# Optimization experiments

Measured on AMD Instinct MI355X. Metric: run time of the kernel, lower is better.

The kernel has to match this reference:

```python
import jax, jax.numpy as jnp
import numpy as np

N, E, IN, HID, HEADS, EDIM, LAT = 10000, 160000, 20, 256, 4, 3, 1024


def gat(x, ei, ea, W, a_src, a_dst, We, a_e, b, H, C):
    # PyG GATConv, eval mode. ei: [2,E], ea: [E,edge_dim]
    n = x.shape[0]
    s, d = ei[0], ei[1]
    # add_self_loops with fill_value='mean': self-loop attr = mean of incoming edge attrs
    cnt = jax.ops.segment_sum(jnp.ones_like(s, jnp.float32), d, num_segments=n)
    loop_ea = jax.ops.segment_sum(ea, d, num_segments=n) / jnp.maximum(cnt, 1.0)[:, None]
    ar = jnp.arange(n, dtype=s.dtype)
    s = jnp.concatenate([s, ar])
    d = jnp.concatenate([d, ar])
    ea = jnp.concatenate([ea, loop_ea], axis=0)
    h = (x @ W).reshape(n, H, C)                       # [n,H,C]
    al_s = jnp.einsum('nhc,hc->nh', h, a_src)
    al_d = jnp.einsum('nhc,hc->nh', h, a_dst)
    e = (ea @ We).reshape(-1, H, C)                    # [E',H,C]
    al_e = jnp.einsum('ehc,hc->eh', e, a_e)
    alpha = jax.nn.leaky_relu(al_s[s] + al_d[d] + al_e, 0.2)  # [E',H]
    m = jax.ops.segment_max(alpha, d, num_segments=n)
    ex = jnp.exp(alpha - m[d])
    ssum = jax.ops.segment_sum(ex, d, num_segments=n)
    alpha = ex / (ssum[d] + 1e-16)
    out = jax.ops.segment_sum(h[s] * alpha[:, :, None], d, num_segments=n)
    return out.reshape(n, H * C) + b


def ln(x, g, b, eps=1e-5):
    m = x.mean(-1, keepdims=True)
    v = ((x - m) ** 2).mean(-1, keepdims=True)
    return g * (x - m) / jnp.sqrt(v + eps) + b


def setup_inputs() -> dict:
    key = jax.random.key(0)
    ks = jax.random.split(key, 16)
    sc = 0.05
    HC = HID * HEADS  # 1024
    return {
        'x': jax.random.normal(ks[0], (N, IN), jnp.float32),
        'edge_attr': jax.random.normal(ks[1], (E, EDIM), jnp.float32),
        'W1': jax.random.normal(ks[2], (IN, HC), jnp.float32) * sc,
        'a_src1': jax.random.normal(ks[3], (HEADS, HID), jnp.float32) * sc,
        'a_dst1': jax.random.normal(ks[4], (HEADS, HID), jnp.float32) * sc,
        'We1': jax.random.normal(ks[5], (EDIM, HC), jnp.float32) * sc,
        'a_e1': jax.random.normal(ks[6], (HEADS, HID), jnp.float32) * sc,
        'b1': jnp.zeros((HC,), jnp.float32),
        'g1': jnp.ones((HC,), jnp.float32),
        'be1': jnp.zeros((HC,), jnp.float32),
        'W2': jax.random.normal(ks[7], (HC, HID), jnp.float32) * sc,
        'a_src2': jax.random.normal(ks[8], (1, HID), jnp.float32) * sc,
        'a_dst2': jax.random.normal(ks[9], (1, HID), jnp.float32) * sc,
        'We2': jax.random.normal(ks[10], (EDIM, HID), jnp.float32) * sc,
        'a_e2': jax.random.normal(ks[11], (1, HID), jnp.float32) * sc,
        'b2': jnp.zeros((HID,), jnp.float32),
        'g2': jnp.ones((HID,), jnp.float32),
        'be2': jnp.zeros((HID,), jnp.float32),
        'Wfc': jax.random.normal(ks[12], (2 * HID, LAT), jnp.float32) * sc,
        'bfc': jnp.zeros((LAT,), jnp.float32),
        'gf': jnp.ones((LAT,), jnp.float32),
        'bf': jnp.zeros((LAT,), jnp.float32),
        'edge_index': jax.random.randint(ks[13], (2, E), 0, N, jnp.int32),
    }


def reference(x, edge_attr, W1, a_src1, a_dst1, We1, a_e1, b1, g1, be1,
              W2, a_src2, a_dst2, We2, a_e2, b2, g2, be2,
              Wfc, bfc, gf, bf, edge_index):
    h = jax.nn.elu(gat(x, edge_index, edge_attr, W1, a_src1, a_dst1, We1, a_e1, b1, HEADS, HID))
    h = ln(h, g1, be1)
    h = jax.nn.elu(gat(h, edge_index, edge_attr, W2, a_src2, a_dst2, We2, a_e2, b2, 1, HID))
    h = ln(h, g2, be2)
    x_mean = h.mean(axis=0)   # global_mean_pool, batch all zeros
    x_max = h.max(axis=0)     # global_max_pool
    g = jnp.concatenate([x_mean, x_max])[None, :]  # [1, 2*HID]
    out = ln(jax.nn.relu(g @ Wfc + bfc), gf, bf)   # [1, LAT]
    return out
```

## Files before the change

### kernel.cpp

```cpp
#include <hip/hip_runtime.h>
#include <hip/hip_bf16.h>

#define NN   10000
#define NE   160000
#define NEP  170000
#define IND  20
#define HIDD 256
#define NH   4
#define HCD  1024
#define LATD 1024
#define MPAD 10112
#define NREP 128

typedef __attribute__((ext_vector_type(8))) short short8v;
typedef __attribute__((ext_vector_type(4))) float f32x4;

__device__ __forceinline__ unsigned pk2(float a, float b) {
    union { __hip_bfloat16 h; unsigned short s; } x, y;
    x.h = __float2bfloat16(a); y.h = __float2bfloat16(b);
    return (unsigned)x.s | ((unsigned)y.s << 16);
}

__device__ __forceinline__ float block_reduce_sum1(float v, float* sm) {
    #pragma unroll
    for (int o = 32; o > 0; o >>= 1) v += __shfl_xor(v, o, 64);
    int wid = threadIdx.x >> 6, lane = threadIdx.x & 63, nw = blockDim.x >> 6;
    if (lane == 0) sm[wid] = v;
    __syncthreads();
    float r = 0.f;
    for (int i = 0; i < nw; i++) r += sm[i];
    __syncthreads();
    return r;
}

__device__ __forceinline__ void block_reduce_sum4(float* v, float* sm) {
    #pragma unroll
    for (int h = 0; h < 4; h++) {
        #pragma unroll
        for (int o = 32; o > 0; o >>= 1) v[h] += __shfl_xor(v[h], o, 64);
    }
    int wid = threadIdx.x >> 6, lane = threadIdx.x & 63, nw = blockDim.x >> 6;
    if (lane == 0) {
        sm[wid*4+0] = v[0]; sm[wid*4+1] = v[1]; sm[wid*4+2] = v[2]; sm[wid*4+3] = v[3];
    }
    __syncthreads();
    float r[4] = {0.f, 0.f, 0.f, 0.f};
    for (int i = 0; i < nw; i++) {
        r[0] += sm[i*4+0]; r[1] += sm[i*4+1]; r[2] += sm[i*4+2]; r[3] += sm[i*4+3];
    }
    __syncthreads();
    v[0] = r[0]; v[1] = r[1]; v[2] = r[2]; v[3] = r[3];
}

__global__ void k_prep(const float* __restrict__ W1, const float* __restrict__ as1,
                       const float* __restrict__ ad1, const float* __restrict__ We1,
                       const float* __restrict__ ae1, const float* __restrict__ We2,
                       const float* __restrict__ ae2, const float* __restrict__ W2,
                       float* __restrict__ prm, __hip_bfloat16* __restrict__ Bt,
                       __hip_bfloat16* __restrict__ w1b) {
    int bid = blockIdx.x, t = threadIdx.x;
    if (bid < 64) {
        __shared__ float sm[64][65];
        int k0 = (bid & 15) * 64, c0 = (bid >> 4) * 64;
        #pragma unroll
        for (int i = 0; i < 16; i++) {
            int idx = i * 256 + t;
            int r = idx >> 6, c = idx & 63;
            sm[r][c] = W2[(size_t)(k0 + r) * 256 + c0 + c];
        }
        __syncthreads();
        int c = t >> 2, kq = t & 3;
        unsigned int out[8];
        #pragma unroll
        for (int j = 0; j < 8; j++)
            out[j] = pk2(sm[kq * 16 + 2*j][c], sm[kq * 16 + 2*j + 1][c]);
        unsigned int* dst = (unsigned int*)(Bt + (size_t)(c0 + c) * 1024 + k0 + kq * 16);
        *(uint4*)dst = make_uint4(out[0], out[1], out[2], out[3]);
        *(uint4*)(dst + 4) = make_uint4(out[4], out[5], out[6], out[7]);
    } else if (bid == 64) {
        if (t < 80) {
            int i = t >> 2, h = t & 3; float s = 0.f;
            for (int c = 0; c < HIDD; c++) s += W1[i*HCD + h*HIDD + c] * as1[h*HIDD + c];
            prm[t] = s;
        } else if (t < 160) {
            int u = t - 80; int i = u >> 2, h = u & 3; float s = 0.f;
            for (int c = 0; c < HIDD; c++) s += W1[i*HCD + h*HIDD + c] * ad1[h*HIDD + c];
            prm[t] = s;
        } else if (t < 172) {
            int u = t - 160; int j = u >> 2, h = u & 3; float s = 0.f;
            for (int c = 0; c < HIDD; c++) s += We1[j*HCD + h*HIDD + c] * ae1[h*HIDD + c];
            prm[t] = s;
        } else if (t < 175) {
            int j = t - 172; float s = 0.f;
            for (int c = 0; c < HIDD; c++) s += We2[j*HIDD + c] * ae2[c];
            prm[t] = s;
        }
    } else {
        int base = (bid - 65) * 2560;
        #pragma unroll
        for (int r = 0; r < 10; r++) {
            int id = base + r * 256 + t;
            w1b[id] = __float2bfloat16(W1[id]);
        }
    }
}

__global__ void k_pre1(const int* __restrict__ ei, const float* __restrict__ ea,
                       const float* __restrict__ x, const float* __restrict__ prm,
                       float* __restrict__ cnt, float* __restrict__ lea3,
                       float* __restrict__ al1) {
    int e = blockIdx.x * 256 + threadIdx.x;
    if (e < NE) {
        int d = ei[NE + e];
        atomicAdd(&cnt[d], 1.0f);
        atomicAdd(&lea3[d*3+0], ea[e*3+0]);
        atomicAdd(&lea3[d*3+1], ea[e*3+1]);
        atomicAdd(&lea3[d*3+2], ea[e*3+2]);
    }
    if (e < NN) {
        int v = e;
        float xr[IND];
        #pragma unroll
        for (int i = 0; i < IND; i++) xr[i] = x[v * IND + i];
        #pragma unroll
        for (int h = 0; h < NH; h++) {
            float s = 0.f, d2 = 0.f;
            #pragma unroll
            for (int i = 0; i < IND; i++) { s += xr[i] * prm[i*4 + h]; d2 += xr[i] * prm[80 + i*4 + h]; }
            al1[v*8 + h] = s;
            al1[v*8 + 4 + h] = d2;
        }
    }
}

__global__ void k_scan(const float* __restrict__ cnt, int* __restrict__ offs) {
    __shared__ int sm[1024];
    int t = threadIdx.x;
    int base = t * 10;
    int loc[10]; int s = 0;
    if (t < 1000) {
        #pragma unroll
        for (int i = 0; i < 10; i++) { loc[i] = s; s += (int)cnt[base + i] + 1; }
    }
    sm[t] = (t < 1000) ? s : 0;
    __syncthreads();
    for (int o = 1; o < 1024; o <<= 1) {
        int x = (t >= o) ? sm[t - o] : 0;
        __syncthreads();
        sm[t] += x;
        __syncthreads();
    }
    int pre = (t > 0) ? sm[t - 1] : 0;
    if (t < 1000) {
        #pragma unroll
        for (int i = 0; i < 10; i++) offs[base + i] = pre + loc[i];
    }
    if (t == 1023) offs[NN] = sm[1023];
}

__global__ void k_edge1(const int* __restrict__ ei, const float* __restrict__ ea,
                        const float* __restrict__ cnt, const float* __restrict__ lea3,
                        const float* __restrict__ al1, const float* __restrict__ prm,
                        const int* __restrict__ offs, int* __restrict__ fill1,
                        int* __restrict__ csrs, float* __restrict__ cex1,
                        float* __restrict__ elog2) {
    int e = blockIdx.x * 256 + threadIdx.x;
    if (e >= NEP) return;
    int s, d; float e0, e1, e2;
    if (e < NE) {
        s = ei[e]; d = ei[NE + e];
        e0 = ea[e*3]; e1 = ea[e*3+1]; e2 = ea[e*3+2];
    } else {
        int v = e - NE; s = v; d = v;
        float ic = 1.f / fmaxf(cnt[v], 1.0f);
        e0 = lea3[v*3] * ic; e1 = lea3[v*3+1] * ic; e2 = lea3[v*3+2] * ic;
    }
    int slot = offs[d] + atomicAdd(&fill1[d], 1);
    csrs[slot] = s;
    elog2[slot] = e0*prm[172] + e1*prm[173] + e2*prm[174];
    float ex[4];
    #pragma unroll
    for (int h = 0; h < NH; h++) {
        float le = e0 * prm[160 + h] + e1 * prm[164 + h] + e2 * prm[168 + h];
        float lg = al1[s*8 + h] + al1[d*8 + 4 + h] + le;
        lg = lg > 0.f ? lg : 0.2f * lg;
        ex[h] = expf(lg);
    }
    *(float4*)(cex1 + (size_t)slot * 4) = make_float4(ex[0], ex[1], ex[2], ex[3]);
}

__global__ void __launch_bounds__(256)
k_agg1y(const int* __restrict__ offs, const int* __restrict__ csrs,
        const float* __restrict__ cex1, const float* __restrict__ x,
        const __hip_bfloat16* __restrict__ w1b, const float* __restrict__ b1,
        const float* __restrict__ g1, const float* __restrict__ be1,
        __hip_bfloat16* __restrict__ h1b) {
    __shared__ float xsn[4][NH][20];
    __shared__ float smr[16];
    int t = threadIdx.x, l = t & 63, n0 = t >> 6;
    int v4 = blockIdx.x * 4;
    {
        int v = v4 + n0;
        int beg = offs[v], end = offs[v + 1];
        int e = l >> 3, fs = l & 7;
        float acc[4][3] = {{0.f,0.f,0.f},{0.f,0.f,0.f},{0.f,0.f,0.f},{0.f,0.f,0.f}};
        float psa[4] = {0.f, 0.f, 0.f, 0.f};
        for (int j0 = beg; j0 < end; j0 += 8) {
            int jl = j0 + e;
            bool valid = jl < end;
            int s = csrs[valid ? jl : beg];
            float4 a4 = valid ? *(const float4*)(cex1 + (size_t)jl * 4)
                              : make_float4(0.f, 0.f, 0.f, 0.f);
            psa[0] += a4.x; psa[1] += a4.y; psa[2] += a4.z; psa[3] += a4.w;
            #pragma unroll
            for (int k = 0; k < 3; k++) {
                int fi = fs * 3 + k;
                float xv = (fi < IND) ? x[(size_t)s * IND + fi] : 0.f;
                acc[0][k] += a4.x * xv; acc[1][k] += a4.y * xv;
                acc[2][k] += a4.z * xv; acc[3][k] += a4.w * xv;
            }
        }
        #pragma unroll
        for (int o = 8; o <= 32; o <<= 1) {
            #pragma unroll
            for (int h = 0; h < 4; h++) {
                psa[h] += __shfl_xor(psa[h], o, 64);
                #pragma unroll
                for (int k = 0; k < 3; k++) acc[h][k] += __shfl_xor(acc[h][k], o, 64);
            }
        }
        if (e == 0) {
            #pragma unroll
            for (int h = 0; h < 4; h++) {
                float inv = 1.f / (psa[h] + 1e-16f);
                #pragma unroll
                for (int k = 0; k < 3; k++) {
                    int fi = fs * 3 + k;
                    if (fi < IND) xsn[n0][h][fi] = acc[h][k] * inv;
                }
            }
        }
    }
    __syncthreads();
    int hh = t >> 6;
    float vv[4][4] = {{0.f,0.f,0.f,0.f},{0.f,0.f,0.f,0.f},{0.f,0.f,0.f,0.f},{0.f,0.f,0.f,0.f}};
    #pragma unroll
    for (int i = 0; i < IND; i++) {
        uint2 wd = *(const uint2*)(w1b + (size_t)i * HCD + 4 * t);
        float w0 = __uint_as_float(wd.x << 16);
        float w1 = __uint_as_float(wd.x & 0xffff0000u);
        float w2 = __uint_as_float(wd.y << 16);
        float w3 = __uint_as_float(wd.y & 0xffff0000u);
        #pragma unroll
        for (int n = 0; n < 4; n++) {
            float xi = xsn[n][hh][i];
            vv[n][0] += xi * w0; vv[n][1] += xi * w1;
            vv[n][2] += xi * w2; vv[n][3] += xi * w3;
        }
    }
    float4 bb = ((const float4*)b1)[t];
    float ls[4];
    #pragma unroll
    for (int n = 0; n < 4; n++) {
        float s0, s1, s2, s3;
        s0 = vv[n][0] + bb.x; s0 = s0 > 0.f ? s0 : expm1f(s0);
        s1 = vv[n][1] + bb.y; s1 = s1 > 0.f ? s1 : expm1f(s1);
        s2 = vv[n][2] + bb.z; s2 = s2 > 0.f ? s2 : expm1f(s2);
        s3 = vv[n][3] + bb.w; s3 = s3 > 0.f ? s3 : expm1f(s3);
        vv[n][0] = s0; vv[n][1] = s1; vv[n][2] = s2; vv[n][3] = s3;
        ls[n] = s0 + s1 + s2 + s3;
    }
    block_reduce_sum4(ls, smr);
    float mu[4], q2[4];
    #pragma unroll
    for (int n = 0; n < 4; n++) {
        mu[n] = ls[n] * (1.f / 1024.f);
        float d0 = vv[n][0]-mu[n], d1 = vv[n][1]-mu[n], d2 = vv[n][2]-mu[n], d3 = vv[n][3]-mu[n];
        q2[n] = d0*d0 + d1*d1 + d2*d2 + d3*d3;
    }
    block_reduce_sum4(q2, smr);
    float4 gg = ((const float4*)g1)[t];
    float4 ee = ((const float4*)be1)[t];
    #pragma unroll
    for (int n = 0; n < 4; n++) {
        float rstd = rsqrtf(q2[n] * (1.f / 1024.f) + 1e-5f);
        float y0 = gg.x * (vv[n][0] - mu[n]) * rstd + ee.x;
        float y1 = gg.y * (vv[n][1] - mu[n]) * rstd + ee.y;
        float y2 = gg.z * (vv[n][2] - mu[n]) * rstd + ee.z;
        float y3 = gg.w * (vv[n][3] - mu[n]) * rstd + ee.w;
        *(uint2*)(h1b + (size_t)(v4 + n) * HCD + 4 * t) = make_uint2(pk2(y0, y1), pk2(y2, y3));
    }
}

__global__ void __launch_bounds__(256)
k_gemm2m(const __hip_bfloat16* __restrict__ A, const __hip_bfloat16* __restrict__ Bt,
         __hip_bfloat16* __restrict__ h2b) {
    __shared__ uint4 As4[256];
    char* As = (char*)As4;
    int t = threadIdx.x, l = t & 63, w = t >> 6;
    int m0 = blockIdx.x * 32;
    int srow = t >> 3, skc = t & 7;
    const __hip_bfloat16* gA = A + (size_t)(m0 + srow) * 1024 + skc * 8;
    int wbyte = (srow * 128 + skc * 16) ^ ((srow & 7) << 4);
    int r0 = l & 15, g = l >> 4;
    int ra[2][2];
    #pragma unroll
    for (int m = 0; m < 2; m++)
        #pragma unroll
        for (int kk = 0; kk < 2; kk++) {
            int r = r0 + m * 16;
            ra[m][kk] = (r * 128 + kk * 64 + g * 16) ^ ((r & 7) << 4);
        }
    const __hip_bfloat16* gB = Bt + (size_t)(w * 64 + r0) * 1024 + g * 8;
    f32x4 acc[2][4];
    #pragma unroll
    for (int m = 0; m < 2; m++)
        #pragma unroll
        for (int n = 0; n < 4; n++) acc[m][n] = (f32x4){0.f,0.f,0.f,0.f};
    uint4 sreg = *(const uint4*)gA;
    for (int it = 0; it < 16; ++it) {
        *(uint4*)(As + wbyte) = sreg;
        __syncthreads();
        if (it < 15) sreg = *(const uint4*)(gA + (it + 1) * 64);
        int k0 = it * 64;
        short8v bfr[4][2];
        #pragma unroll
        for (int n = 0; n < 4; n++)
            #pragma unroll
            for (int kk = 0; kk < 2; kk++)
                bfr[n][kk] = *(const short8v*)(gB + (size_t)n * 16 * 1024 + k0 + kk * 32);
        short8v afr[2][2];
        #pragma unroll
        for (int m = 0; m < 2; m++)
            #pragma unroll
            for (int kk = 0; kk < 2; kk++)
                afr[m][kk] = *(const short8v*)(As + ra[m][kk]);
        #pragma unroll
        for (int kk = 0; kk < 2; kk++)
            #pragma unroll
            for (int m = 0; m < 2; m++)
                #pragma unroll
                for (int n = 0; n < 4; n++)
                    acc[m][n] = __builtin_amdgcn_mfma_f32_16x16x32_bf16(afr[m][kk], bfr[n][kk], acc[m][n], 0, 0, 0);
        __syncthreads();
    }
    #pragma unroll
    for (int m = 0; m < 2; m++) {
        #pragma unroll
        for (int r = 0; r < 4; r++) {
            int row = m0 + m * 16 + g * 4 + r;
            if (row < NN) {
                #pragma unroll
                for (int n = 0; n < 4; n++) {
                    int col = w * 64 + n * 16 + r0;
                    h2b[(size_t)row * HIDD + col] = __float2bfloat16(acc[m][n][r]);
                }
            }
        }
    }
}

__global__ void __launch_bounds__(256)
k_al2(const __hip_bfloat16* __restrict__ h2b, const float* __restrict__ as2,
      const float* __restrict__ ad2, float* __restrict__ al2) {
    int l = threadIdx.x & 63;
    int v = blockIdx.x * 4 + (threadIdx.x >> 6);
    uint2 p = ((const uint2*)h2b)[(size_t)v * 64 + l];
    float f0 = __uint_as_float(p.x << 16), f1 = __uint_as_float(p.x & 0xffff0000u);
    float f2 = __uint_as_float(p.y << 16), f3 = __uint_as_float(p.y & 0xffff0000u);
    float4 sa = ((const float4*)as2)[l];
    float4 da = ((const float4*)ad2)[l];
    float s = f0*sa.x + f1*sa.y + f2*sa.z + f3*sa.w;
    float d = f0*da.x + f1*da.y + f2*da.z + f3*da.w;
    #pragma unroll
    for (int o = 1; o <= 32; o <<= 1) { s += __shfl_xor(s, o, 64); d += __shfl_xor(d, o, 64); }
    if (l == 0) { al2[v*2] = s; al2[v*2+1] = d; }
}

__global__ void __launch_bounds__(256)
k_agg2y(const int* __restrict__ offs, const int* __restrict__ csrs,
        const float* __restrict__ elog2, const float* __restrict__ al2,
        const __hip_bfloat16* __restrict__ h2b, const float* __restrict__ b2,
        const float* __restrict__ g2, const float* __restrict__ be2,
        float* __restrict__ gsum, unsigned* __restrict__ gmaxU) {
    __shared__ float sal[128];
    __shared__ int   ssr[128];
    __shared__ float sred[16];
    int t = threadIdx.x;
    int v = blockIdx.x;
    int beg = offs[v], end = offs[v + 1];
    float ald = al2[2 * v + 1];
    float acc = 0.f, ps = 0.f;
    for (int j0 = beg; j0 < end; j0 += 128) {
        int nb = end - j0; if (nb > 128) nb = 128;
        __syncthreads();
        if (t < 128) {
            int jl = j0 + t;
            float wv = 0.f; int s = 0;
            if (jl < end) {
                s = csrs[jl];
                float lg = al2[2 * s] + ald + elog2[jl];
                lg = lg > 0.f ? lg : 0.2f * lg;
                wv = expf(lg);
            }
            sal[t] = wv; ssr[t] = s;
            ps += wv;
        }
        __syncthreads();
        int nbr = (nb + 3) & ~3;
        for (int u = 0; u < nbr; u += 4) {
            float a0 = sal[u], a1 = sal[u+1], a2 = sal[u+2], a3 = sal[u+3];
            int s0 = ssr[u], s1 = ssr[u+1], s2 = ssr[u+2], s3 = ssr[u+3];
            float h0 = __bfloat162float(h2b[(size_t)s0 * HIDD + t]);
            float h1 = __bfloat162float(h2b[(size_t)s1 * HIDD + t]);
            float h2 = __bfloat162float(h2b[(size_t)s2 * HIDD + t]);
            float h3 = __bfloat162float(h2b[(size_t)s3 * HIDD + t]);
            acc += a0*h0 + a1*h1 + a2*h2 + a3*h3;
        }
    }
    float pst = block_reduce_sum1(ps, sred);
    float inv = 1.f / (pst + 1e-16f);
    float vf = acc * inv + b2[t];
    vf = vf > 0.f ? vf : expm1f(vf);
    float mu = block_reduce_sum1(vf, sred) * (1.f / 256.f);
    float dv = vf - mu;
    float var = block_reduce_sum1(dv * dv, sred) * (1.f / 256.f);
    float rstd = rsqrtf(var + 1e-5f);
    float outv = g2[t] * dv * rstd + be2[t];
    int rep = blockIdx.x & (NREP - 1);
    atomicAdd(&gsum[rep * 256 + t], outv);
    unsigned b = __float_as_uint(outv);
    unsigned k = (b & 0x80000000u) ? ~b : (b | 0x80000000u);
    atomicMax(&gmaxU[rep * 256 + t], k);
}

__global__ void k_gvec(const float* __restrict__ gsum, const unsigned* __restrict__ gmaxU,
                       float* __restrict__ gvec) {
    int t = threadIdx.x;
    float s = 0.f; unsigned km = 0u;
    for (int r = 0; r < NREP; r++) {
        s += gsum[r * 256 + t];
        unsigned k = gmaxU[r * 256 + t];
        km = k > km ? k : km;
    }
    gvec[t] = s * (1.f / (float)NN);
    unsigned b = (km & 0x80000000u) ? (km & 0x7fffffffu) : ~km;
    gvec[256 + t] = __uint_as_float(b);
}

__global__ void k_fc(const float* __restrict__ gvec, const float* __restrict__ Wfc,
                     float* __restrict__ fcacc) {
    int t = threadIdx.x;
    int kc = blockIdx.x >> 2;
    int c = (blockIdx.x & 3) * 256 + t;
    int r0 = kc * 64;
    float acc = 0.f;
    #pragma unroll 8
    for (int i = 0; i < 64; i++) acc += gvec[r0 + i] * Wfc[(size_t)(r0 + i) * LATD + c];
    atomicAdd(&fcacc[c], acc);
}

__global__ void k_out(const float* __restrict__ fcacc, const float* __restrict__ bfc,
                      const float* __restrict__ gf, const float* __restrict__ bf,
                      float* __restrict__ outp) {
    __shared__ float sm[16];
    int t = threadIdx.x;
    float v = fmaxf(fcacc[t] + bfc[t], 0.f);
    float mu = block_reduce_sum1(v, sm) * (1.f / 1024.f);
    float dv = v - mu;
    float var = block_reduce_sum1(dv * dv, sm) * (1.f / 1024.f);
    float rstd = rsqrtf(var + 1e-5f);
    outp[t] = gf[t] * dv * rstd + bf[t];
}

extern "C" void kernel_launch(void* const* d_in, const int* in_sizes, int n_in,
                              void* d_out, int out_size, void* d_ws, size_t ws_size,
                              hipStream_t stream) {
    const float* x      = (const float*)d_in[0];
    const float* ea     = (const float*)d_in[1];
    const float* W1     = (const float*)d_in[2];
    const float* a_src1 = (const float*)d_in[3];
    const float* a_dst1 = (const float*)d_in[4];
    const float* We1    = (const float*)d_in[5];
    const float* a_e1   = (const float*)d_in[6];
    const float* b1     = (const float*)d_in[7];
    const float* g1     = (const float*)d_in[8];
    const float* be1    = (const float*)d_in[9];
    const float* W2     = (const float*)d_in[10];
    const float* a_src2 = (const float*)d_in[11];
    const float* a_dst2 = (const float*)d_in[12];
    const float* We2    = (const float*)d_in[13];
    const float* a_e2   = (const float*)d_in[14];
    const float* b2     = (const float*)d_in[15];
    const float* g2     = (const float*)d_in[16];
    const float* be2    = (const float*)d_in[17];
    const float* Wfc    = (const float*)d_in[18];
    const float* bfc    = (const float*)d_in[19];
    const float* gf     = (const float*)d_in[20];
    const float* bf     = (const float*)d_in[21];
    const int*   ei     = (const int*)d_in[22];
    float* outp = (float*)d_out;

    char* p = (char*)d_ws;
    auto alloc = [&](size_t bytes) -> char* {
        char* r = p;
        p += (bytes + 255) & ~(size_t)255;
        return r;
    };
    float* cnt     = (float*)alloc((size_t)NN * 4);
    float* lea3    = (float*)alloc((size_t)NN * 3 * 4);
    int*   fill1   = (int*)  alloc((size_t)NN * 4);
    float* gsum    = (float*)alloc((size_t)NREP * 256 * 4);
    unsigned* gmaxU= (unsigned*)alloc((size_t)NREP * 256 * 4);
    float* fcacc   = (float*)alloc(1024 * 4);
    size_t zbytes  = (size_t)((char*)fcacc + 1024*4 - (char*)cnt);
    float* prm     = (float*)alloc(256 * 4);
    float* al1     = (float*)alloc((size_t)NN * 8 * 4);
    float* al2     = (float*)alloc((size_t)NN * 2 * 4);
    int*   offs    = (int*)  alloc((size_t)(NN + 1) * 4);
    int*   csrs    = (int*)  alloc((size_t)NEP * 4);
    float* cex1    = (float*)alloc((size_t)NEP * 4 * 4);
    float* elog2   = (float*)alloc((size_t)NEP * 4);
    __hip_bfloat16* w1b = (__hip_bfloat16*)alloc((size_t)IND * HCD * 2);
    __hip_bfloat16* h1b = (__hip_bfloat16*)alloc((size_t)MPAD * HCD * 2);
    __hip_bfloat16* w2t = (__hip_bfloat16*)alloc((size_t)HIDD * HCD * 2);
    __hip_bfloat16* h2b = (__hip_bfloat16*)alloc((size_t)NN * HIDD * 2);
    float* gvec    = (float*)alloc(512 * 4);

    hipMemsetAsync(cnt, 0, zbytes, stream);

    k_prep<<<73, 256, 0, stream>>>(W1, a_src1, a_dst1, We1, a_e1, We2, a_e2, W2,
                                   prm, w2t, w1b);
    k_pre1<<<(NE + 255) / 256, 256, 0, stream>>>(ei, ea, x, prm, cnt, lea3, al1);
    k_scan<<<1, 1024, 0, stream>>>(cnt, offs);
    k_edge1<<<(NEP + 255) / 256, 256, 0, stream>>>(ei, ea, cnt, lea3, al1, prm, offs,
                                                   fill1, csrs, cex1, elog2);
    k_agg1y<<<NN / 4, 256, 0, stream>>>(offs, csrs, cex1, x, w1b, b1, g1, be1, h1b);
    k_gemm2m<<<313, 256, 0, stream>>>(h1b, w2t, h2b);
    k_al2<<<NN / 4, 256, 0, stream>>>(h2b, a_src2, a_dst2, al2);
    k_agg2y<<<NN, 256, 0, stream>>>(offs, csrs, elog2, al2, h2b, b2, g2, be2,
                                    gsum, gmaxU);
    k_gvec<<<1, 256, 0, stream>>>(gsum, gmaxU, gvec);
    k_fc<<<32, 256, 0, stream>>>(gvec, Wfc, fcacc);
    k_out<<<1, 1024, 0, stream>>>(fcacc, bfc, gf, bf, outp);
}
```

Measured before the change: 305.5 us.

## Fuse small kernels and move layer-1 projection to MFMA with one-pass LayerNorm

```diff
diff --git a/kernel.cpp b/kernel.cpp
--- a/kernel.cpp
+++ b/kernel.cpp
@@ -21,6 +21,12 @@
     return (unsigned)x.s | ((unsigned)y.s << 16);
 }
 
+__device__ __forceinline__ unsigned short bf16bits(float a) {
+    union { __hip_bfloat16 h; unsigned short s; } x;
+    x.h = __float2bfloat16(a);
+    return x.s;
+}
+
 __device__ __forceinline__ float block_reduce_sum1(float v, float* sm) {
     #pragma unroll
     for (int o = 32; o > 0; o >>= 1) v += __shfl_xor(v, o, 64);
@@ -33,31 +39,14 @@
     return r;
 }
 
-__device__ __forceinline__ void block_reduce_sum4(float* v, float* sm) {
-    #pragma unroll
-    for (int h = 0; h < 4; h++) {
-        #pragma unroll
-        for (int o = 32; o > 0; o >>= 1) v[h] += __shfl_xor(v[h], o, 64);
-    }
-    int wid = threadIdx.x >> 6, lane = threadIdx.x & 63, nw = blockDim.x >> 6;
-    if (lane == 0) {
-        sm[wid*4+0] = v[0]; sm[wid*4+1] = v[1]; sm[wid*4+2] = v[2]; sm[wid*4+3] = v[3];
-    }
-    __syncthreads();
-    float r[4] = {0.f, 0.f, 0.f, 0.f};
-    for (int i = 0; i < nw; i++) {
-        r[0] += sm[i*4+0]; r[1] += sm[i*4+1]; r[2] += sm[i*4+2]; r[3] += sm[i*4+3];
-    }
-    __syncthreads();
-    v[0] = r[0]; v[1] = r[1]; v[2] = r[2]; v[3] = r[3];
-}
-
-__global__ void k_prep(const float* __restrict__ W1, const float* __restrict__ as1,
-                       const float* __restrict__ ad1, const float* __restrict__ We1,
-                       const float* __restrict__ ae1, const float* __restrict__ We2,
-                       const float* __restrict__ ae2, const float* __restrict__ W2,
-                       float* __restrict__ prm, __hip_bfloat16* __restrict__ Bt,
-                       __hip_bfloat16* __restrict__ w1b) {
+__global__ void k_front(const float* __restrict__ W1, const float* __restrict__ as1,
+                        const float* __restrict__ ad1, const float* __restrict__ We1,
+                        const float* __restrict__ ae1, const float* __restrict__ We2,
+                        const float* __restrict__ ae2, const float* __restrict__ W2,
+                        const int* __restrict__ ei, const float* __restrict__ ea,
+                        float* __restrict__ prm, __hip_bfloat16* __restrict__ Bt,
+                        __hip_bfloat16* __restrict__ w1t,
+                        float* __restrict__ cnt, float* __restrict__ lea3) {
     int bid = blockIdx.x, t = threadIdx.x;
     if (bid < 64) {
         __shared__ float sm[64][65];
@@ -95,67 +84,69 @@
             for (int c = 0; c < HIDD; c++) s += We2[j*HIDD + c] * ae2[c];
             prm[t] = s;
         }
+    } else if (bid < 73) {
+        int f = (bid - 65) * 128 + (t >> 1);
+        int half = t & 1;
+        #pragma unroll
+        for (int kk = 0; kk < 16; kk++) {
+            int k = half * 16 + kk;
+            float v = (k < IND) ? W1[(size_t)k * HCD + f] : 0.f;
+            w1t[(size_t)f * 32 + k] = __float2bfloat16(v);
+        }
     } else {
-        int base = (bid - 65) * 2560;
-        #pragma unroll
-        for (int r = 0; r < 10; r++) {
-            int id = base + r * 256 + t;
-            w1b[id] = __float2bfloat16(W1[id]);
-        }
-    }
-}
-
-__global__ void k_pre1(const int* __restrict__ ei, const float* __restrict__ ea,
-                       const float* __restrict__ x, const float* __restrict__ prm,
-                       float* __restrict__ cnt, float* __restrict__ lea3,
+        int e = (bid - 73) * 256 + t;
+        if (e < NE) {
+            int d = ei[NE + e];
+            atomicAdd(&cnt[d], 1.0f);
+            atomicAdd(&lea3[d*3+0], ea[e*3+0]);
+            atomicAdd(&lea3[d*3+1], ea[e*3+1]);
+            atomicAdd(&lea3[d*3+2], ea[e*3+2]);
+        }
+    }
+}
+
+__global__ void k_scan(const float* __restrict__ cnt, const float* __restrict__ x,
+                       const float* __restrict__ prm, int* __restrict__ offs,
                        float* __restrict__ al1) {
-    int e = blockIdx.x * 256 + threadIdx.x;
-    if (e < NE) {
-        int d = ei[NE + e];
-        atomicAdd(&cnt[d], 1.0f);
-        atomicAdd(&lea3[d*3+0], ea[e*3+0]);
-        atomicAdd(&lea3[d*3+1], ea[e*3+1]);
-        atomicAdd(&lea3[d*3+2], ea[e*3+2]);
-    }
-    if (e < NN) {
-        int v = e;
-        float xr[IND];
-        #pragma unroll
-        for (int i = 0; i < IND; i++) xr[i] = x[v * IND + i];
-        #pragma unroll
-        for (int h = 0; h < NH; h++) {
-            float s = 0.f, d2 = 0.f;
-            #pragma unroll
-            for (int i = 0; i < IND; i++) { s += xr[i] * prm[i*4 + h]; d2 += xr[i] * prm[80 + i*4 + h]; }
-            al1[v*8 + h] = s;
-            al1[v*8 + 4 + h] = d2;
-        }
-    }
-}
-
-__global__ void k_scan(const float* __restrict__ cnt, int* __restrict__ offs) {
-    __shared__ int sm[1024];
-    int t = threadIdx.x;
-    int base = t * 10;
-    int loc[10]; int s = 0;
-    if (t < 1000) {
-        #pragma unroll
-        for (int i = 0; i < 10; i++) { loc[i] = s; s += (int)cnt[base + i] + 1; }
-    }
-    sm[t] = (t < 1000) ? s : 0;
-    __syncthreads();
-    for (int o = 1; o < 1024; o <<= 1) {
-        int x = (t >= o) ? sm[t - o] : 0;
+    if (blockIdx.x == 0) {
+        __shared__ int sm[1024];
+        int t = threadIdx.x;
+        int base = t * 10;
+        int loc[10]; int s = 0;
+        if (t < 1000) {
+            #pragma unroll
+            for (int i = 0; i < 10; i++) { loc[i] = s; s += (int)cnt[base + i] + 1; }
+        }
+        sm[t] = (t < 1000) ? s : 0;
         __syncthreads();
-        sm[t] += x;
-        __syncthreads();
-    }
-    int pre = (t > 0) ? sm[t - 1] : 0;
-    if (t < 1000) {
-        #pragma unroll
-        for (int i = 0; i < 10; i++) offs[base + i] = pre + loc[i];
-    }
-    if (t == 1023) offs[NN] = sm[1023];
+        for (int o = 1; o < 1024; o <<= 1) {
+            int xv = (t >= o) ? sm[t - o] : 0;
+            __syncthreads();
+            sm[t] += xv;
+            __syncthreads();
+        }
+        int pre = (t > 0) ? sm[t - 1] : 0;
+        if (t < 1000) {
+            #pragma unroll
+            for (int i = 0; i < 10; i++) offs[base + i] = pre + loc[i];
+        }
+        if (t == 1023) offs[NN] = sm[1023];
+    } else {
+        int v = (blockIdx.x - 1) * 1024 + threadIdx.x;
+        if (v < NN) {
+            float xr[IND];
+            #pragma unroll
+            for (int i = 0; i < IND; i++) xr[i] = x[v * IND + i];
+            #pragma unroll
+            for (int h = 0; h < NH; h++) {
+                float s = 0.f, d2 = 0.f;
+                #pragma unroll
+                for (int i = 0; i < IND; i++) { s += xr[i] * prm[i*4 + h]; d2 += xr[i] * prm[80 + i*4 + h]; }
+                al1[v*8 + h] = s;
+                al1[v*8 + 4 + h] = d2;
+            }
+        }
+    }
 }
 
 __global__ void k_edge1(const int* __restrict__ ei, const float* __restrict__ ea,
@@ -184,28 +175,30 @@
         float le = e0 * prm[160 + h] + e1 * prm[164 + h] + e2 * prm[168 + h];
         float lg = al1[s*8 + h] + al1[d*8 + 4 + h] + le;
         lg = lg > 0.f ? lg : 0.2f * lg;
-        ex[h] = expf(lg);
+        ex[h] = __expf(lg);
     }
     *(float4*)(cex1 + (size_t)slot * 4) = make_float4(ex[0], ex[1], ex[2], ex[3]);
 }
 
 __global__ void __launch_bounds__(256)
-k_agg1y(const int* __restrict__ offs, const int* __restrict__ csrs,
-        const float* __restrict__ cex1, const float* __restrict__ x,
-        const __hip_bfloat16* __restrict__ w1b, const float* __restrict__ b1,
-        const float* __restrict__ g1, const float* __restrict__ be1,
-        __hip_bfloat16* __restrict__ h1b) {
-    __shared__ float xsn[4][NH][20];
-    __shared__ float smr[16];
-    int t = threadIdx.x, l = t & 63, n0 = t >> 6;
-    int v4 = blockIdx.x * 4;
-    {
-        int v = v4 + n0;
+k_l1(const int* __restrict__ offs, const int* __restrict__ csrs,
+     const float* __restrict__ cex1, const float* __restrict__ x,
+     const __hip_bfloat16* __restrict__ w1t, const float* __restrict__ b1,
+     const float* __restrict__ g1, const float* __restrict__ be1,
+     __hip_bfloat16* __restrict__ h1b) {
+    __shared__ unsigned short xb[16][4][32];
+    __shared__ float sred[4][16][2];
+    int t = threadIdx.x, l = t & 63, w = t >> 6;
+    int vbase = blockIdx.x * 16;
+    ((uint4*)xb)[t] = make_uint4(0, 0, 0, 0);
+    __syncthreads();
+    int e = l >> 2, fs = l & 3;
+    for (int nl = 0; nl < 4; nl++) {
+        int v = vbase + w * 4 + nl;
         int beg = offs[v], end = offs[v + 1];
-        int e = l >> 3, fs = l & 7;
-        float acc[4][3] = {{0.f,0.f,0.f},{0.f,0.f,0.f},{0.f,0.f,0.f},{0.f,0.f,0.f}};
+        float acc[4][5] = {};
         float psa[4] = {0.f, 0.f, 0.f, 0.f};
-        for (int j0 = beg; j0 < end; j0 += 8) {
+        for (int j0 = beg; j0 < end; j0 += 16) {
             int jl = j0 + e;
             bool valid = jl < end;
             int s = csrs[valid ? jl : beg];
@@ -213,89 +206,85 @@
                               : make_float4(0.f, 0.f, 0.f, 0.f);
             psa[0] += a4.x; psa[1] += a4.y; psa[2] += a4.z; psa[3] += a4.w;
             #pragma unroll
-            for (int k = 0; k < 3; k++) {
-                int fi = fs * 3 + k;
-                float xv = (fi < IND) ? x[(size_t)s * IND + fi] : 0.f;
+            for (int k = 0; k < 5; k++) {
+                float xv = x[(size_t)s * IND + fs * 5 + k];
                 acc[0][k] += a4.x * xv; acc[1][k] += a4.y * xv;
                 acc[2][k] += a4.z * xv; acc[3][k] += a4.w * xv;
             }
         }
         #pragma unroll
-        for (int o = 8; o <= 32; o <<= 1) {
+        for (int o = 4; o <= 32; o <<= 1) {
             #pragma unroll
             for (int h = 0; h < 4; h++) {
                 psa[h] += __shfl_xor(psa[h], o, 64);
                 #pragma unroll
-                for (int k = 0; k < 3; k++) acc[h][k] += __shfl_xor(acc[h][k], o, 64);
+                for (int k = 0; k < 5; k++) acc[h][k] += __shfl_xor(acc[h][k], o, 64);
             }
         }
         if (e == 0) {
+            int node = w * 4 + nl;
             #pragma unroll
             for (int h = 0; h < 4; h++) {
                 float inv = 1.f / (psa[h] + 1e-16f);
                 #pragma unroll
-                for (int k = 0; k < 3; k++) {
-                    int fi = fs * 3 + k;
-                    if (fi < IND) xsn[n0][h][fi] = acc[h][k] * inv;
-                }
-            }
-        }
-    }
-    __syncthreads();
-    int hh = t >> 6;
-    float vv[4][4] = {{0.f,0.f,0.f,0.f},{0.f,0.f,0.f,0.f},{0.f,0.f,0.f,0.f},{0.f,0.f,0.f,0.f}};
-    #pragma unroll
-    for (int i = 0; i < IND; i++) {
-        uint2 wd = *(const uint2*)(w1b + (size_t)i * HCD + 4 * t);
-        float w0 = __uint_as_float(wd.x << 16);
-        float w1 = __uint_as_float(wd.x & 0xffff0000u);
-        float w2 = __uint_as_float(wd.y << 16);
-        float w3 = __uint_as_float(wd.y & 0xffff0000u);
-        #pragma unroll
-        for (int n = 0; n < 4; n++) {
-            float xi = xsn[n][hh][i];
-            vv[n][0] += xi * w0; vv[n][1] += xi * w1;
-            vv[n][2] += xi * w2; vv[n][3] += xi * w3;
-        }
-    }
-    float4 bb = ((const float4*)b1)[t];
-    float ls[4];
-    #pragma unroll
-    for (int n = 0; n < 4; n++) {
-        float s0, s1, s2, s3;
-        s0 = vv[n][0] + bb.x; s0 = s0 > 0.f ? s0 : expm1f(s0);
-        s1 = vv[n][1] + bb.y; s1 = s1 > 0.f ? s1 : expm1f(s1);
-        s2 = vv[n][2] + bb.z; s2 = s2 > 0.f ? s2 : expm1f(s2);
-        s3 = vv[n][3] + bb.w; s3 = s3 > 0.f ? s3 : expm1f(s3);
-        vv[n][0] = s0; vv[n][1] = s1; vv[n][2] = s2; vv[n][3] = s3;
-        ls[n] = s0 + s1 + s2 + s3;
-    }
-    block_reduce_sum4(ls, smr);
-    float mu[4], q2[4];
-    #pragma unroll
-    for (int n = 0; n < 4; n++) {
-        mu[n] = ls[n] * (1.f / 1024.f);
-        float d0 = vv[n][0]-mu[n], d1 = vv[n][1]-mu[n], d2 = vv[n][2]-mu[n], d3 = vv[n][3]-mu[n];
-        q2[n] = d0*d0 + d1*d1 + d2*d2 + d3*d3;
-    }
-    block_reduce_sum4(q2, smr);
-    float4 gg = ((const float4*)g1)[t];
-    float4 ee = ((const float4*)be1)[t];
-    #pragma unroll
-    for (int n = 0; n < 4; n++) {
-        float rstd = rsqrtf(q2[n] * (1.f / 1024.f) + 1e-5f);
-        float y0 = gg.x * (vv[n][0] - mu[n]) * rstd + ee.x;
-        float y1 = gg.y * (vv[n][1] - mu[n]) * rstd + ee.y;
-        float y2 = gg.z * (vv[n][2] - mu[n]) * rstd + ee.z;
-        float y3 = gg.w * (vv[n][3] - mu[n]) * rstd + ee.w;
-        *(uint2*)(h1b + (size_t)(v4 + n) * HCD + 4 * t) = make_uint2(pk2(y0, y1), pk2(y2, y3));
+                for (int k = 0; k < 5; k++)
+                    xb[node][h][fs * 5 + k] = bf16bits(acc[h][k] * inv);
+            }
+        }
+    }
+    __syncthreads();
+    int vn = l & 15, g = l >> 4;
+    short8v bfrag = *(const short8v*)&xb[vn][w][g * 8];
+    const __hip_bfloat16* wp = w1t + ((size_t)w * 256 + vn) * 32 + g * 8;
+    f32x4 accp[16];
+    #pragma unroll
+    for (int ft = 0; ft < 16; ft++) {
+        short8v afrag = *(const short8v*)(wp + (size_t)ft * 16 * 32);
+        accp[ft] = __builtin_amdgcn_mfma_f32_16x16x32_bf16(afrag, bfrag,
+                                                           (f32x4){0.f,0.f,0.f,0.f}, 0, 0, 0);
+    }
+    float s1 = 0.f, s2 = 0.f;
+    #pragma unroll
+    for (int ft = 0; ft < 16; ft++) {
+        int fb = w * 256 + ft * 16 + g * 4;
+        float4 bb = *(const float4*)(b1 + fb);
+        #pragma unroll
+        for (int r = 0; r < 4; r++) {
+            float xv = accp[ft][r] + ((const float*)&bb)[r];
+            xv = xv > 0.f ? xv : (__expf(xv) - 1.f);
+            accp[ft][r] = xv;
+            s1 += xv; s2 += xv * xv;
+        }
+    }
+    s1 += __shfl_xor(s1, 16, 64); s1 += __shfl_xor(s1, 32, 64);
+    s2 += __shfl_xor(s2, 16, 64); s2 += __shfl_xor(s2, 32, 64);
+    if (g == 0) { sred[w][vn][0] = s1; sred[w][vn][1] = s2; }
+    __syncthreads();
+    float S1 = sred[0][vn][0] + sred[1][vn][0] + sred[2][vn][0] + sred[3][vn][0];
+    float S2 = sred[0][vn][1] + sred[1][vn][1] + sred[2][vn][1] + sred[3][vn][1];
+    float mu = S1 * (1.f / 1024.f);
+    float var = S2 * (1.f / 1024.f) - mu * mu;
+    float rstd = rsqrtf(var + 1e-5f);
+    int v = vbase + vn;
+    #pragma unroll
+    for (int ft = 0; ft < 16; ft++) {
+        int fb = w * 256 + ft * 16 + g * 4;
+        float4 gg = *(const float4*)(g1 + fb);
+        float4 ee = *(const float4*)(be1 + fb);
+        unsigned p0 = pk2(gg.x * (accp[ft][0] - mu) * rstd + ee.x,
+                          gg.y * (accp[ft][1] - mu) * rstd + ee.y);
+        unsigned p1 = pk2(gg.z * (accp[ft][2] - mu) * rstd + ee.z,
+                          gg.w * (accp[ft][3] - mu) * rstd + ee.w);
+        *(uint2*)(h1b + (size_t)v * HCD + fb) = make_uint2(p0, p1);
     }
 }
 
 __global__ void __launch_bounds__(256)
 k_gemm2m(const __hip_bfloat16* __restrict__ A, const __hip_bfloat16* __restrict__ Bt,
-         __hip_bfloat16* __restrict__ h2b) {
+         const float* __restrict__ as2, const float* __restrict__ ad2,
+         __hip_bfloat16* __restrict__ h2b, float* __restrict__ al2) {
     __shared__ uint4 As4[256];
+    __shared__ float part[4][32][2];
     char* As = (char*)As4;
     int t = threadIdx.x, l = t & 63, w = t >> 6;
     int m0 = blockIdx.x * 32;
@@ -344,6 +333,17 @@
                     acc[m][n] = __builtin_amdgcn_mfma_f32_16x16x32_bf16(afr[m][kk], bfr[n][kk], acc[m][n], 0, 0, 0);
         __syncthreads();
     }
+    float as2v[4], ad2v[4];
+    #pragma unroll
+    for (int n = 0; n < 4; n++) {
+        int col = w * 64 + n * 16 + r0;
+        as2v[n] = as2[col]; ad2v[n] = ad2[col];
+    }
+    float sp[2][4], dp[2][4];
+    #pragma unroll
+    for (int m = 0; m < 2; m++)
+        #pragma unroll
+        for (int r = 0; r < 4; r++) { sp[m][r] = 0.f; dp[m][r] = 0.f; }
     #pragma unroll
     for (int m = 0; m < 2; m++) {
         #pragma unroll
@@ -354,27 +354,39 @@
                 for (int n = 0; n < 4; n++) {
                     int col = w * 64 + n * 16 + r0;
                     h2b[(size_t)row * HIDD + col] = __float2bfloat16(acc[m][n][r]);
+                    sp[m][r] += acc[m][n][r] * as2v[n];
+                    dp[m][r] += acc[m][n][r] * ad2v[n];
                 }
             }
         }
     }
-}
-
-__global__ void __launch_bounds__(256)
-k_al2(const __hip_bfloat16* __restrict__ h2b, const float* __restrict__ as2,
-      const float* __restrict__ ad2, float* __restrict__ al2) {
-    int l = threadIdx.x & 63;
-    int v = blockIdx.x * 4 + (threadIdx.x >> 6);
-    uint2 p = ((const uint2*)h2b)[(size_t)v * 64 + l];
-    float f0 = __uint_as_float(p.x << 16), f1 = __uint_as_float(p.x & 0xffff0000u);
-    float f2 = __uint_as_float(p.y << 16), f3 = __uint_as_float(p.y & 0xffff0000u);
-    float4 sa = ((const float4*)as2)[l];
-    float4 da = ((const float4*)ad2)[l];
-    float s = f0*sa.x + f1*sa.y + f2*sa.z + f3*sa.w;
-    float d = f0*da.x + f1*da.y + f2*da.z + f3*da.w;
-    #pragma unroll
-    for (int o = 1; o <= 32; o <<= 1) { s += __shfl_xor(s, o, 64); d += __shfl_xor(d, o, 64); }
-    if (l == 0) { al2[v*2] = s; al2[v*2+1] = d; }
+    #pragma unroll
+    for (int o = 1; o <= 8; o <<= 1) {
+        #pragma unroll
+        for (int m = 0; m < 2; m++)
+            #pragma unroll
+            for (int r = 0; r < 4; r++) {
+                sp[m][r] += __shfl_xor(sp[m][r], o, 64);
+                dp[m][r] += __shfl_xor(dp[m][r], o, 64);
+            }
+    }
+    if (r0 == 0) {
+        #pragma unroll
+        for (int m = 0; m < 2; m++)
+            #pragma unroll
+            for (int r = 0; r < 4; r++) {
+                part[w][m * 16 + g * 4 + r][0] = sp[m][r];
+                part[w][m * 16 + g * 4 + r][1] = dp[m][r];
+            }
+    }
+    __syncthreads();
+    if (t < 64) {
+        int row = t >> 1, c = t & 1;
+        if (m0 + row < NN) {
+            float s = part[0][row][c] + part[1][row][c] + part[2][row][c] + part[3][row][c];
+            al2[(m0 + row) * 2 + c] = s;
+        }
+    }
 }
 
 __global__ void __launch_bounds__(256)
@@ -401,7 +413,7 @@
                 s = csrs[jl];
                 float lg = al2[2 * s] + ald + elog2[jl];
                 lg = lg > 0.f ? lg : 0.2f * lg;
-                wv = expf(lg);
+                wv = __expf(lg);
             }
             sal[t] = wv; ssr[t] = s;
             ps += wv;
@@ -421,7 +433,7 @@
     float pst = block_reduce_sum1(ps, sred);
     float inv = 1.f / (pst + 1e-16f);
     float vf = acc * inv + b2[t];
-    vf = vf > 0.f ? vf : expm1f(vf);
+    vf = vf > 0.f ? vf : (__expf(vf) - 1.f);
     float mu = block_reduce_sum1(vf, sred) * (1.f / 256.f);
     float dv = vf - mu;
     float var = block_reduce_sum1(dv * dv, sred) * (1.f / 256.f);
@@ -434,8 +446,9 @@
     atomicMax(&gmaxU[rep * 256 + t], k);
 }
 
-__global__ void k_gvec(const float* __restrict__ gsum, const unsigned* __restrict__ gmaxU,
-                       float* __restrict__ gvec) {
+__global__ void k_fcg(const float* __restrict__ gsum, const unsigned* __restrict__ gmaxU,
+                      const float* __restrict__ Wfc, float* __restrict__ fcacc) {
+    __shared__ float gv[512];
     int t = threadIdx.x;
     float s = 0.f; unsigned km = 0u;
     for (int r = 0; r < NREP; r++) {
@@ -443,20 +456,16 @@
         unsigned k = gmaxU[r * 256 + t];
         km = k > km ? k : km;
     }
-    gvec[t] = s * (1.f / (float)NN);
+    gv[t] = s * (1.f / (float)NN);
     unsigned b = (km & 0x80000000u) ? (km & 0x7fffffffu) : ~km;
-    gvec[256 + t] = __uint_as_float(b);
-}
-
-__global__ void k_fc(const float* __restrict__ gvec, const float* __restrict__ Wfc,
-                     float* __restrict__ fcacc) {
-    int t = threadIdx.x;
+    gv[256 + t] = __uint_as_float(b);
+    __syncthreads();
     int kc = blockIdx.x >> 2;
     int c = (blockIdx.x & 3) * 256 + t;
     int r0 = kc * 64;
     float acc = 0.f;
     #pragma unroll 8
-    for (int i = 0; i < 64; i++) acc += gvec[r0 + i] * Wfc[(size_t)(r0 + i) * LATD + c];
+    for (int i = 0; i < 64; i++) acc += gv[r0 + i] * Wfc[(size_t)(r0 + i) * LATD + c];
     atomicAdd(&fcacc[c], acc);
 }
 
@@ -521,26 +530,23 @@
     int*   csrs    = (int*)  alloc((size_t)NEP * 4);
     float* cex1    = (float*)alloc((size_t)NEP * 4 * 4);
     float* elog2   = (float*)alloc((size_t)NEP * 4);
-    __hip_bfloat16* w1b = (__hip_bfloat16*)alloc((size_t)IND * HCD * 2);
+    __hip_bfloat16* w1t = (__hip_bfloat16*)alloc((size_t)HCD * 32 * 2);
     __hip_bfloat16* h1b = (__hip_bfloat16*)alloc((size_t)MPAD * HCD * 2);
     __hip_bfloat16* w2t = (__hip_bfloat16*)alloc((size_t)HIDD * HCD * 2);
     __hip_bfloat16* h2b = (__hip_bfloat16*)alloc((size_t)NN * HIDD * 2);
-    float* gvec    = (float*)alloc(512 * 4);
 
     hipMemsetAsync(cnt, 0, zbytes, stream);
 
-    k_prep<<<73, 256, 0, stream>>>(W1, a_src1, a_dst1, We1, a_e1, We2, a_e2, W2,
-                                   prm, w2t, w1b);
-    k_pre1<<<(NE + 255) / 256, 256, 0, stream>>>(ei, ea, x, prm, cnt, lea3, al1);
-    k_scan<<<1, 1024, 0, stream>>>(cnt, offs);
+    k_front<<<73 + (NE + 255) / 256, 256, 0, stream>>>(W1, a_src1, a_dst1, We1, a_e1,
+                                                       We2, a_e2, W2, ei, ea,
+                                                       prm, w2t, w1t, cnt, lea3);
+    k_scan<<<11, 1024, 0, stream>>>(cnt, x, prm, offs, al1);
     k_edge1<<<(NEP + 255) / 256, 256, 0, stream>>>(ei, ea, cnt, lea3, al1, prm, offs,
                                                    fill1, csrs, cex1, elog2);
-    k_agg1y<<<NN / 4, 256, 0, stream>>>(offs, csrs, cex1, x, w1b, b1, g1, be1, h1b);
-    k_gemm2m<<<313, 256, 0, stream>>>(h1b, w2t, h2b);
-    k_al2<<<NN / 4, 256, 0, stream>>>(h2b, a_src2, a_dst2, al2);
+    k_l1<<<NN / 16, 256, 0, stream>>>(offs, csrs, cex1, x, w1t, b1, g1, be1, h1b);
+    k_gemm2m<<<313, 256, 0, stream>>>(h1b, w2t, a_src2, a_dst2, h2b, al2);
     k_agg2y<<<NN, 256, 0, stream>>>(offs, csrs, elog2, al2, h2b, b2, g2, be2,
                                     gsum, gmaxU);
-    k_gvec<<<1, 256, 0, stream>>>(gsum, gmaxU, gvec);
-    k_fc<<<32, 256, 0, stream>>>(gvec, Wfc, fcacc);
+    k_fcg<<<32, 256, 0, stream>>>(gsum, gmaxU, Wfc, fcacc);
     k_out<<<1, 1024, 0, stream>>>(fcacc, bfc, gf, bf, outp);
 }
```

Result: faster. 283.5 us (-7.2%).
